# Optimization experiments

Measured on AMD Instinct MI355X. Metric: run time of the kernel, lower is better.

The kernel has to match this reference:

```python
import jax, jax.numpy as jnp
import numpy as np

B, S, D = 128, 512, 768          # batch, seq_len, token_dim
NH, HD = 8, 96                    # num_heads, head_dim = sentence_dim/num_heads
HID = 4 * HD                      # hidden_dim = 384


def setup_inputs() -> dict:
    key = jax.random.key(0)
    ks = jax.random.split(key, 9)
    token_embeddings = jax.random.normal(ks[0], (B, S, D), dtype=jnp.float32)
    # variable-length attention mask (1 for real tokens, 0 for padding)
    lengths = jax.random.randint(ks[1], (B,), S // 2, S + 1)
    attention_mask = (jnp.arange(S)[None, :] < lengths[:, None]).astype(jnp.float32)
    s = 0.02
    P  = jax.random.normal(ks[2], (NH, HD, D),   dtype=jnp.float32) * s
    bP = jnp.zeros((NH, HD), dtype=jnp.float32)
    W1 = jax.random.normal(ks[3], (NH, HID, HD), dtype=jnp.float32) * s
    b1 = jnp.zeros((NH, HID), dtype=jnp.float32)
    W2 = jax.random.normal(ks[4], (NH, HD, HID), dtype=jnp.float32) * s
    b2 = jnp.zeros((NH, HD), dtype=jnp.float32)
    return {"token_embeddings": token_embeddings, "attention_mask": attention_mask,
            "P": P, "bP": bP, "W1": W1, "b1": b1, "W2": W2, "b2": b2}


def reference(token_embeddings, attention_mask, P, bP, W1, b1, W2, b2):
    # per-head projection: H_i = P_i(H)           -> (nh, B, S, HD)
    Hi = jnp.einsum('bsd,ihd->ibsh', token_embeddings, P) + bP[:, None, None, :]
    # scores: W2(relu(W1(H_i)))                   -> (nh, B, S, HD)
    A = jnp.einsum('ibsf,ihf->ibsh',
                   jax.nn.relu(jnp.einsum('ibsh,ifh->ibsf', Hi, W1) + b1[:, None, None, :]),
                   W2) + b2[:, None, None, :]
    # masked softmax over sequence dim (log(mask) adds -inf on padding)
    log_mask = jnp.log(attention_mask)[None, :, :, None]  # (1, B, S, 1)
    A = jax.nn.softmax(A + log_mask, axis=2)
    # weighted sum over tokens                    -> (nh, B, HD)
    v = jnp.sum(Hi * A, axis=2)
    # concat heads: (B, nh*HD) = (B, 768)
    pooled = jnp.transpose(v, (1, 0, 2)).reshape(token_embeddings.shape[0], NH * HD)
    return pooled
```

## Files before the change

### kernel.cpp

```cpp
#include <hip/hip_runtime.h>
#include <stdint.h>


typedef short bf16x8 __attribute__((ext_vector_type(8)));
typedef float f32x4 __attribute__((ext_vector_type(4)));

struct alignas(8) us4 { unsigned short x, y, z, w; };

__device__ __forceinline__ unsigned short f32_to_bf16(float f) {
  union { float f; uint32_t u; } v; v.f = f;
  uint32_t u = v.u;
  uint32_t r = (u + 0x7fffu + ((u >> 16) & 1u)) >> 16;
  return (unsigned short)r;
}

__device__ __forceinline__ float bf16_to_f32(unsigned short h) {
  union { uint32_t u; float f; } v; v.u = ((uint32_t)h) << 16;
  return v.f;
}

__device__ __forceinline__ uint32_t pack_bf16_trunc(float lo, float hi) {
  union { float f; uint32_t u; } a, b; a.f = lo; b.f = hi;
  return __builtin_amdgcn_perm(b.u, a.u, 0x07060302u);
}

__device__ __forceinline__ void g2l16(const unsigned short* g, unsigned short* l) {
  __builtin_amdgcn_global_load_lds((__attribute__((address_space(1))) void*)g,
                                   (__attribute__((address_space(3))) void*)l,
                                   16, 0, 0);
}


#define N_X   50331648
#define N_P   589824
#define N_W1  294912
#define N_W2  294912
#define N_HI  50331648


__global__ __launch_bounds__(256) void cast_f32_bf16(
    const float* __restrict__ src, unsigned short* __restrict__ dst, int n4) {
  int idx = blockIdx.x * 256 + threadIdx.x;
  if (idx >= n4) return;
  float4 v = ((const float4*)src)[idx];
  us4 o;
  o.x = f32_to_bf16(v.x);
  o.y = f32_to_bf16(v.y);
  o.z = f32_to_bf16(v.z);
  o.w = f32_to_bf16(v.w);
  ((us4*)dst)[idx] = o;
}


__global__ __launch_bounds__(256) void gemm_hi(
    const unsigned short* __restrict__ Xbf,
    const unsigned short* __restrict__ Pbf,
    const float* __restrict__ bP,
    unsigned short* __restrict__ Hi) {
  __shared__ __align__(16) unsigned short As[128 * 32];
  __shared__ __align__(16) unsigned short Bs[128 * 32];

  const int tid = threadIdx.x;
  const int w = tid >> 6;
  const int lane = tid & 63;
  const int r = lane & 15;
  const int q = lane >> 4;
  const int bn = blockIdx.x;
  const int bm = blockIdx.y;
  const int wr = w >> 1, wc = w & 1;

  f32x4 acc[4][4];
#pragma unroll
  for (int a = 0; a < 4; ++a)
#pragma unroll
    for (int c = 0; c < 4; ++c) acc[a][c] = (f32x4){0.f, 0.f, 0.f, 0.f};

  const int ldr = lane >> 2;
  const int ldc = (lane & 3) * 8;
  const unsigned short* Abase = Xbf + (size_t)(bm * 128) * 768 + ldc;
  const unsigned short* Bbase = Pbf + (size_t)(bn * 128) * 768 + ldc;

  for (int k0 = 0; k0 < 768; k0 += 32) {
    __syncthreads();
    g2l16(Abase + (size_t)(w * 16 + ldr) * 768 + k0, &As[w * 512]);
    g2l16(Abase + (size_t)(64 + w * 16 + ldr) * 768 + k0, &As[(4 + w) * 512]);
    g2l16(Bbase + (size_t)(w * 16 + ldr) * 768 + k0, &Bs[w * 512]);
    g2l16(Bbase + (size_t)(64 + w * 16 + ldr) * 768 + k0, &Bs[(4 + w) * 512]);
    __syncthreads();

    bf16x8 af[4], bfr[4];
#pragma unroll
    for (int t = 0; t < 4; ++t)
      af[t] = *(const bf16x8*)&As[(wr * 64 + t * 16 + r) * 32 + q * 8];
#pragma unroll
    for (int t = 0; t < 4; ++t)
      bfr[t] = *(const bf16x8*)&Bs[(wc * 64 + t * 16 + r) * 32 + q * 8];
#pragma unroll
    for (int mt = 0; mt < 4; ++mt)
#pragma unroll
      for (int nt = 0; nt < 4; ++nt)
        acc[mt][nt] = __builtin_amdgcn_mfma_f32_16x16x32_bf16(
            af[mt], bfr[nt], acc[mt][nt], 0, 0, 0);
  }

  const int bb = bm >> 2;
  const int sb = (bm & 3) * 128 + wr * 64;
#pragma unroll
  for (int nt = 0; nt < 4; ++nt) {
    const int n0 = bn * 128 + wc * 64 + nt * 16;
    const int hd = n0 / 96;
    const int h = n0 - hd * 96 + r;
    const float bias = bP[n0 + r];
    unsigned short* obase = Hi + (size_t)(hd * 128 + bb) * 512 * 96 + h;
#pragma unroll
    for (int mt = 0; mt < 4; ++mt) {
#pragma unroll
      for (int rg = 0; rg < 4; ++rg) {
        const int s = sb + mt * 16 + q * 4 + rg;
        obase[(size_t)s * 96] = f32_to_bf16(acc[mt][nt][rg] + bias);
      }
    }
  }
}


__global__ __launch_bounds__(256, 2) void mlp_logits(
    const unsigned short* __restrict__ Hi,
    const unsigned short* __restrict__ W1bf,
    const unsigned short* __restrict__ W2bf,
    const float* __restrict__ b1,
    const float* __restrict__ b2,
    unsigned short* __restrict__ Alog) {
  __shared__ __align__(16) unsigned short Ys[128 * 96];
  __shared__ __align__(16) unsigned short Ws[96 * 96];
  __shared__ __align__(16) unsigned short Fs[128 * 104];
  __shared__ __align__(16) float b1s[384];
  __shared__ __align__(16) float b2s[96];

  const int x = blockIdx.x;
  const int c = x & 3;
  const int b = (x >> 2) & 127;
  const int hd = x >> 9;

  const int tid = threadIdx.x;
  const int w = tid >> 6;
  const int lane = tid & 63;
  const int r = lane & 15;
  const int q = lane >> 4;

  const unsigned short* ysrc = Hi + ((size_t)(hd * 128 + b) * 512 + c * 128) * 96;
#pragma unroll
  for (int it = 0; it < 6; ++it)
    g2l16(ysrc + (size_t)((it * 4 + w) * 64 + lane) * 8, &Ys[(it * 4 + w) * 512]);

  if (tid < 96) b2s[tid] = b2[hd * 96 + tid];
  for (int i = tid; i < 384; i += 256) b1s[i] = b1[hd * 384 + i];

  f32x4 acc3[2][6];
#pragma unroll
  for (int sp = 0; sp < 2; ++sp)
#pragma unroll
    for (int nt = 0; nt < 6; ++nt) acc3[sp][nt] = (f32x4){0.f, 0.f, 0.f, 0.f};

  for (int ph = 0; ph < 4; ++ph) {
    __syncthreads();
    const unsigned short* w1src = W1bf + ((size_t)hd * 384 + ph * 96) * 96;
#pragma unroll
    for (int it = 0; it < 4; ++it)
      g2l16(w1src + (size_t)((it * 4 + w) * 64 + lane) * 8, &Ws[(it * 4 + w) * 512]);
    if (w < 2)
      g2l16(w1src + (size_t)((16 + w) * 64 + lane) * 8, &Ws[(16 + w) * 512]);
    __syncthreads();

    f32x4 acc2[6][2];
#pragma unroll
    for (int ft = 0; ft < 6; ++ft)
#pragma unroll
      for (int sp = 0; sp < 2; ++sp) acc2[ft][sp] = (f32x4){0.f, 0.f, 0.f, 0.f};
#pragma unroll
    for (int kb = 0; kb < 3; ++kb) {
      bf16x8 bfrg[2];
#pragma unroll
      for (int sp = 0; sp < 2; ++sp)
        bfrg[sp] = *(const bf16x8*)&Ys[((w * 2 + sp) * 16 + r) * 96 + kb * 32 + q * 8];
#pragma unroll
      for (int ft = 0; ft < 6; ++ft) {
        bf16x8 afrg = *(const bf16x8*)&Ws[(ft * 16 + r) * 96 + kb * 32 + q * 8];
#pragma unroll
        for (int sp = 0; sp < 2; ++sp)
          acc2[ft][sp] = __builtin_amdgcn_mfma_f32_16x16x32_bf16(
              afrg, bfrg[sp], acc2[ft][sp], 0, 0, 0);
      }
    }
#pragma unroll
    for (int ft = 0; ft < 6; ++ft) {
      float4 bv = *(const float4*)&b1s[ph * 96 + ft * 16 + q * 4];
#pragma unroll
      for (int sp = 0; sp < 2; ++sp) {
        const int s = (w * 2 + sp) * 16 + r;
        float v0 = fmaxf(acc2[ft][sp][0] + bv.x, 0.f);
        float v1 = fmaxf(acc2[ft][sp][1] + bv.y, 0.f);
        float v2 = fmaxf(acc2[ft][sp][2] + bv.z, 0.f);
        float v3 = fmaxf(acc2[ft][sp][3] + bv.w, 0.f);
        uint2 pk;
        pk.x = pack_bf16_trunc(v0, v1);
        pk.y = pack_bf16_trunc(v2, v3);
        *(uint2*)((uint32_t*)&Fs[0] + s * 52 + ft * 8 + q * 2) = pk;
      }
    }
    __syncthreads();

    const unsigned short* w2src = W2bf + (size_t)hd * 96 * 384 + ph * 96;
#pragma unroll
    for (int it = 0; it < 4; ++it) {
      const int ch = (it * 4 + w) * 64 + lane;
      const int kb = ch / 384;
      const int rem = ch - kb * 384;
      g2l16(w2src + (size_t)(rem >> 2) * 384 + kb * 32 + (rem & 3) * 8,
            &Ws[(it * 4 + w) * 512]);
    }
    if (w < 2) {
      const int ch = (16 + w) * 64 + lane;
      const int kb = ch / 384;
      const int rem = ch - kb * 384;
      g2l16(w2src + (size_t)(rem >> 2) * 384 + kb * 32 + (rem & 3) * 8,
            &Ws[(16 + w) * 512]);
    }
    __syncthreads();

#pragma unroll
    for (int kb = 0; kb < 3; ++kb) {
      bf16x8 afrg[2];
#pragma unroll
      for (int sp = 0; sp < 2; ++sp)
        afrg[sp] = *(const bf16x8*)&Fs[((w * 2 + sp) * 16 + r) * 104 + kb * 32 + q * 8];
#pragma unroll
      for (int nt = 0; nt < 6; ++nt) {
        bf16x8 bfrg = *(const bf16x8*)&Ws[(kb * 96 + nt * 16 + r) * 32 + q * 8];
#pragma unroll
        for (int sp = 0; sp < 2; ++sp)
          acc3[sp][nt] = __builtin_amdgcn_mfma_f32_16x16x32_bf16(
              afrg[sp], bfrg, acc3[sp][nt], 0, 0, 0);
      }
    }
  }

  unsigned short* aout = Alog + ((size_t)(hd * 128 + b) * 512 + c * 128) * 96;
#pragma unroll
  for (int nt = 0; nt < 6; ++nt) {
    const int h = nt * 16 + r;
    const float bias = b2s[h];
#pragma unroll
    for (int sp = 0; sp < 2; ++sp) {
#pragma unroll
      for (int rg = 0; rg < 4; ++rg) {
        const int s = (w * 2 + sp) * 16 + q * 4 + rg;
        aout[(size_t)s * 96 + h] = f32_to_bf16(acc3[sp][nt][rg] + bias);
      }
    }
  }
}


__global__ __launch_bounds__(384) void softpool(
    const unsigned short* __restrict__ Hi,
    const unsigned short* __restrict__ Alog,
    const float* __restrict__ mask,
    float* __restrict__ out) {
  __shared__ float bias[512];
  __shared__ float redl[32][96];
  __shared__ float redv[32][96];
  __shared__ float mfin[96];

  const int x = blockIdx.x;
  const int hd = x >> 7;
  const int b = x & 127;
  const int tid = threadIdx.x;
  const int g = tid / 12;
  const int t12 = tid - g * 12;
  const int h8 = t12 * 8;

  for (int s = tid; s < 512; s += 384)
    bias[s] = mask[b * 512 + s] > 0.5f ? 0.f : -1e30f;
  __syncthreads();

  const unsigned short* abase = Alog + (size_t)x * 512 * 96;
  const unsigned short* hbase = Hi + (size_t)x * 512 * 96;

  float m[8];
#pragma unroll
  for (int j = 0; j < 8; ++j) m[j] = -3e30f;
#pragma unroll
  for (int it = 0; it < 16; ++it) {
    const int s = g * 16 + it;
    bf16x8 a = *(const bf16x8*)&abase[(size_t)s * 96 + h8];
    const float bs = bias[s];
#pragma unroll
    for (int j = 0; j < 8; ++j)
      m[j] = fmaxf(m[j], bf16_to_f32((unsigned short)a[j]) + bs);
  }
#pragma unroll
  for (int j = 0; j < 8; ++j) redl[g][h8 + j] = m[j];
  __syncthreads();
  if (tid < 96) {
    float mm = -3e30f;
#pragma unroll
    for (int gg = 0; gg < 32; ++gg) mm = fmaxf(mm, redl[gg][tid]);
    mfin[tid] = mm;
  }
  __syncthreads();
  float mf[8];
#pragma unroll
  for (int j = 0; j < 8; ++j) mf[j] = mfin[h8 + j];
  __syncthreads();

  float l[8], v[8];
#pragma unroll
  for (int j = 0; j < 8; ++j) { l[j] = 0.f; v[j] = 0.f; }
#pragma unroll
  for (int it = 0; it < 16; ++it) {
    const int s = g * 16 + it;
    bf16x8 a = *(const bf16x8*)&abase[(size_t)s * 96 + h8];
    bf16x8 hv = *(const bf16x8*)&hbase[(size_t)s * 96 + h8];
    const float bs = bias[s];
#pragma unroll
    for (int j = 0; j < 8; ++j) {
      float e = __expf(bf16_to_f32((unsigned short)a[j]) + bs - mf[j]);
      l[j] += e;
      v[j] += e * bf16_to_f32((unsigned short)hv[j]);
    }
  }
#pragma unroll
  for (int j = 0; j < 8; ++j) {
    redl[g][h8 + j] = l[j];
    redv[g][h8 + j] = v[j];
  }
  __syncthreads();
  if (tid < 96) {
    float ls = 0.f, vs = 0.f;
#pragma unroll
    for (int gg = 0; gg < 32; ++gg) { ls += redl[gg][tid]; vs += redv[gg][tid]; }
    out[b * 768 + hd * 96 + tid] = vs / ls;
  }
}


extern "C" void kernel_launch(void* const* d_in, const int* in_sizes, int n_in,
                              void* d_out, int out_size, void* d_ws, size_t ws_size,
                              hipStream_t stream) {
  const float* X    = (const float*)d_in[0];
  const float* mask = (const float*)d_in[1];
  const float* P    = (const float*)d_in[2];
  const float* bP   = (const float*)d_in[3];
  const float* W1   = (const float*)d_in[4];
  const float* b1   = (const float*)d_in[5];
  const float* W2   = (const float*)d_in[6];
  const float* b2   = (const float*)d_in[7];
  float* out = (float*)d_out;
  (void)in_sizes; (void)n_in; (void)out_size; (void)ws_size;

  unsigned short* Xbf  = (unsigned short*)d_ws;
  unsigned short* Pbf  = Xbf + N_X;
  unsigned short* W1bf = Pbf + N_P;
  unsigned short* W2bf = W1bf + N_W1;
  unsigned short* Hi   = W2bf + N_W2;
  unsigned short* Alog = Hi + N_HI;

  cast_f32_bf16<<<N_X / 4 / 256, 256, 0, stream>>>(X, Xbf, N_X / 4);
  cast_f32_bf16<<<N_P / 4 / 256, 256, 0, stream>>>(P, Pbf, N_P / 4);
  cast_f32_bf16<<<N_W1 / 4 / 256, 256, 0, stream>>>(W1, W1bf, N_W1 / 4);
  cast_f32_bf16<<<N_W2 / 4 / 256, 256, 0, stream>>>(W2, W2bf, N_W2 / 4);

  gemm_hi<<<dim3(6, 512), 256, 0, stream>>>(Xbf, Pbf, bP, Hi);
  mlp_logits<<<8 * 128 * 4, 256, 0, stream>>>(Hi, W1bf, W2bf, b1, b2, Alog);
  softpool<<<8 * 128, 384, 0, stream>>>(Hi, Alog, mask, out);
}
```

Measured before the change: 581.0 us.

## Keep MLP intermediate in registers via ds_bpermute, drop LDS staging and syncs

Rewrites mlp_logits so the Hi tile, W1 and W2 fragments are loaded directly from global memory into registers rather than staged through shared memory. The ReLU hidden activations are passed from the first MFMA output layout into the second MFMA input layout with ds_bpermute lane shuffles instead of an LDS round trip. This removes all __syncthreads and shared memory from the kernel and raises the occupancy hint to 3 blocks per CU. The output store is also reworked to write packed 4-element bf16 vectors along the head dim. In exchange, weights are re-read from global/L2 by every wave, with more, smaller loads and higher register pressure.

```diff
diff --git a/kernel.cpp b/kernel.cpp
--- a/kernel.cpp
+++ b/kernel.cpp
@@ -124,19 +124,13 @@
 }
 
 
-__global__ __launch_bounds__(256, 2) void mlp_logits(
+__global__ __launch_bounds__(256, 3) void mlp_logits(
     const unsigned short* __restrict__ Hi,
     const unsigned short* __restrict__ W1bf,
     const unsigned short* __restrict__ W2bf,
     const float* __restrict__ b1,
     const float* __restrict__ b2,
     unsigned short* __restrict__ Alog) {
-  __shared__ __align__(16) unsigned short Ys[128 * 96];
-  __shared__ __align__(16) unsigned short Ws[96 * 96];
-  __shared__ __align__(16) unsigned short Fs[128 * 104];
-  __shared__ __align__(16) float b1s[384];
-  __shared__ __align__(16) float b2s[96];
-
   const int x = blockIdx.x;
   const int c = x & 3;
   const int b = (x >> 2) & 127;
@@ -148,13 +142,23 @@
   const int r = lane & 15;
   const int q = lane >> 4;
 
-  const unsigned short* ysrc = Hi + ((size_t)(hd * 128 + b) * 512 + c * 128) * 96;
-#pragma unroll
-  for (int it = 0; it < 6; ++it)
-    g2l16(ysrc + (size_t)((it * 4 + w) * 64 + lane) * 8, &Ys[(it * 4 + w) * 512]);
-
-  if (tid < 96) b2s[tid] = b2[hd * 96 + tid];
-  for (int i = tid; i < 384; i += 256) b1s[i] = b1[hd * 384 + i];
+  const unsigned short* ybase = Hi + ((size_t)(hd * 128 + b) * 512 + c * 128) * 96;
+  const unsigned short* w1h = W1bf + (size_t)hd * 384 * 96;
+  const unsigned short* w2h = W2bf + (size_t)hd * 96 * 384;
+  const float* b1h = b1 + hd * 384;
+  const float* b2h = b2 + hd * 96;
+
+  bf16x8 yf[2][3];
+#pragma unroll
+  for (int sp = 0; sp < 2; ++sp)
+#pragma unroll
+    for (int kb = 0; kb < 3; ++kb)
+      yf[sp][kb] =
+          *(const bf16x8*)&ybase[((w * 2 + sp) * 16 + r) * 96 + kb * 32 + q * 8];
+
+  const int vaddr_a = (((lane >> 4) & 1) * 32 + r) * 4;
+  const int vaddr_b = vaddr_a + 64;
+  const bool hiq = lane >= 32;
 
   f32x4 acc3[2][6];
 #pragma unroll
@@ -163,100 +167,77 @@
     for (int nt = 0; nt < 6; ++nt) acc3[sp][nt] = (f32x4){0.f, 0.f, 0.f, 0.f};
 
   for (int ph = 0; ph < 4; ++ph) {
-    __syncthreads();
-    const unsigned short* w1src = W1bf + ((size_t)hd * 384 + ph * 96) * 96;
-#pragma unroll
-    for (int it = 0; it < 4; ++it)
-      g2l16(w1src + (size_t)((it * 4 + w) * 64 + lane) * 8, &Ws[(it * 4 + w) * 512]);
-    if (w < 2)
-      g2l16(w1src + (size_t)((16 + w) * 64 + lane) * 8, &Ws[(16 + w) * 512]);
-    __syncthreads();
-
-    f32x4 acc2[6][2];
-#pragma unroll
-    for (int ft = 0; ft < 6; ++ft)
-#pragma unroll
-      for (int sp = 0; sp < 2; ++sp) acc2[ft][sp] = (f32x4){0.f, 0.f, 0.f, 0.f};
-#pragma unroll
-    for (int kb = 0; kb < 3; ++kb) {
-      bf16x8 bfrg[2];
-#pragma unroll
-      for (int sp = 0; sp < 2; ++sp)
-        bfrg[sp] = *(const bf16x8*)&Ys[((w * 2 + sp) * 16 + r) * 96 + kb * 32 + q * 8];
-#pragma unroll
-      for (int ft = 0; ft < 6; ++ft) {
-        bf16x8 afrg = *(const bf16x8*)&Ws[(ft * 16 + r) * 96 + kb * 32 + q * 8];
-#pragma unroll
-        for (int sp = 0; sp < 2; ++sp)
-          acc2[ft][sp] = __builtin_amdgcn_mfma_f32_16x16x32_bf16(
-              afrg, bfrg[sp], acc2[ft][sp], 0, 0, 0);
+#pragma unroll
+    for (int kb2 = 0; kb2 < 3; ++kb2) {
+      uint32_t PX[2][2], PY[2][2];
+#pragma unroll
+      for (int fh = 0; fh < 2; ++fh) {
+        const int ft = kb2 * 2 + fh;
+        const int frow = ph * 96 + ft * 16 + r;
+        f32x4 a2[2];
+        a2[0] = (f32x4){0.f, 0.f, 0.f, 0.f};
+        a2[1] = (f32x4){0.f, 0.f, 0.f, 0.f};
+#pragma unroll
+        for (int kb = 0; kb < 3; ++kb) {
+          bf16x8 w1f = *(const bf16x8*)&w1h[(size_t)frow * 96 + kb * 32 + q * 8];
+#pragma unroll
+          for (int sp = 0; sp < 2; ++sp)
+            a2[sp] = __builtin_amdgcn_mfma_f32_16x16x32_bf16(w1f, yf[sp][kb],
+                                                             a2[sp], 0, 0, 0);
+        }
+        const float4 bv = *(const float4*)&b1h[ph * 96 + ft * 16 + q * 4];
+#pragma unroll
+        for (int sp = 0; sp < 2; ++sp) {
+          float v0 = fmaxf(a2[sp][0] + bv.x, 0.f);
+          float v1 = fmaxf(a2[sp][1] + bv.y, 0.f);
+          float v2 = fmaxf(a2[sp][2] + bv.z, 0.f);
+          float v3 = fmaxf(a2[sp][3] + bv.w, 0.f);
+          PX[fh][sp] = pack_bf16_trunc(v0, v1);
+          PY[fh][sp] = pack_bf16_trunc(v2, v3);
+        }
+      }
+      bf16x8 w2f[6];
+#pragma unroll
+      for (int nt = 0; nt < 6; ++nt)
+        w2f[nt] = *(const bf16x8*)&w2h[(size_t)(nt * 16 + r) * 384 + ph * 96 +
+                                       kb2 * 32 + q * 8];
+#pragma unroll
+      for (int sp = 0; sp < 2; ++sp) {
+        union { bf16x8 v; uint32_t d[4]; } bb;
+        uint32_t t0, t1;
+        t0 = (uint32_t)__builtin_amdgcn_ds_bpermute(vaddr_a, (int)PX[0][sp]);
+        t1 = (uint32_t)__builtin_amdgcn_ds_bpermute(vaddr_a, (int)PX[1][sp]);
+        bb.d[0] = hiq ? t1 : t0;
+        t0 = (uint32_t)__builtin_amdgcn_ds_bpermute(vaddr_a, (int)PY[0][sp]);
+        t1 = (uint32_t)__builtin_amdgcn_ds_bpermute(vaddr_a, (int)PY[1][sp]);
+        bb.d[1] = hiq ? t1 : t0;
+        t0 = (uint32_t)__builtin_amdgcn_ds_bpermute(vaddr_b, (int)PX[0][sp]);
+        t1 = (uint32_t)__builtin_amdgcn_ds_bpermute(vaddr_b, (int)PX[1][sp]);
+        bb.d[2] = hiq ? t1 : t0;
+        t0 = (uint32_t)__builtin_amdgcn_ds_bpermute(vaddr_b, (int)PY[0][sp]);
+        t1 = (uint32_t)__builtin_amdgcn_ds_bpermute(vaddr_b, (int)PY[1][sp]);
+        bb.d[3] = hiq ? t1 : t0;
+#pragma unroll
+        for (int nt = 0; nt < 6; ++nt)
+          acc3[sp][nt] = __builtin_amdgcn_mfma_f32_16x16x32_bf16(
+              w2f[nt], bb.v, acc3[sp][nt], 0, 0, 0);
       }
     }
-#pragma unroll
-    for (int ft = 0; ft < 6; ++ft) {
-      float4 bv = *(const float4*)&b1s[ph * 96 + ft * 16 + q * 4];
-#pragma unroll
-      for (int sp = 0; sp < 2; ++sp) {
-        const int s = (w * 2 + sp) * 16 + r;
-        float v0 = fmaxf(acc2[ft][sp][0] + bv.x, 0.f);
-        float v1 = fmaxf(acc2[ft][sp][1] + bv.y, 0.f);
-        float v2 = fmaxf(acc2[ft][sp][2] + bv.z, 0.f);
-        float v3 = fmaxf(acc2[ft][sp][3] + bv.w, 0.f);
-        uint2 pk;
-        pk.x = pack_bf16_trunc(v0, v1);
-        pk.y = pack_bf16_trunc(v2, v3);
-        *(uint2*)((uint32_t*)&Fs[0] + s * 52 + ft * 8 + q * 2) = pk;
-      }
-    }
-    __syncthreads();
-
-    const unsigned short* w2src = W2bf + (size_t)hd * 96 * 384 + ph * 96;
-#pragma unroll
-    for (int it = 0; it < 4; ++it) {
-      const int ch = (it * 4 + w) * 64 + lane;
-      const int kb = ch / 384;
-      const int rem = ch - kb * 384;
-      g2l16(w2src + (size_t)(rem >> 2) * 384 + kb * 32 + (rem & 3) * 8,
-            &Ws[(it * 4 + w) * 512]);
-    }
-    if (w < 2) {
-      const int ch = (16 + w) * 64 + lane;
-      const int kb = ch / 384;
-      const int rem = ch - kb * 384;
-      g2l16(w2src + (size_t)(rem >> 2) * 384 + kb * 32 + (rem & 3) * 8,
-            &Ws[(16 + w) * 512]);
-    }
-    __syncthreads();
-
-#pragma unroll
-    for (int kb = 0; kb < 3; ++kb) {
-      bf16x8 afrg[2];
-#pragma unroll
-      for (int sp = 0; sp < 2; ++sp)
-        afrg[sp] = *(const bf16x8*)&Fs[((w * 2 + sp) * 16 + r) * 104 + kb * 32 + q * 8];
-#pragma unroll
-      for (int nt = 0; nt < 6; ++nt) {
-        bf16x8 bfrg = *(const bf16x8*)&Ws[(kb * 96 + nt * 16 + r) * 32 + q * 8];
-#pragma unroll
-        for (int sp = 0; sp < 2; ++sp)
-          acc3[sp][nt] = __builtin_amdgcn_mfma_f32_16x16x32_bf16(
-              afrg[sp], bfrg, acc3[sp][nt], 0, 0, 0);
-      }
-    }
   }
 
   unsigned short* aout = Alog + ((size_t)(hd * 128 + b) * 512 + c * 128) * 96;
 #pragma unroll
   for (int nt = 0; nt < 6; ++nt) {
-    const int h = nt * 16 + r;
-    const float bias = b2s[h];
+    const float4 bv = *(const float4*)&b2h[nt * 16 + q * 4];
 #pragma unroll
     for (int sp = 0; sp < 2; ++sp) {
-#pragma unroll
-      for (int rg = 0; rg < 4; ++rg) {
-        const int s = (w * 2 + sp) * 16 + q * 4 + rg;
-        aout[(size_t)s * 96 + h] = f32_to_bf16(acc3[sp][nt][rg] + bias);
-      }
+      const int s = (w * 2 + sp) * 16 + r;
+      uint2 pk;
+      pk.x = (uint32_t)f32_to_bf16(acc3[sp][nt][0] + bv.x) |
+             ((uint32_t)f32_to_bf16(acc3[sp][nt][1] + bv.y) << 16);
+      pk.y = (uint32_t)f32_to_bf16(acc3[sp][nt][2] + bv.z) |
+             ((uint32_t)f32_to_bf16(acc3[sp][nt][3] + bv.w) << 16);
+      *(uint2*)&aout[(size_t)s * 96 + nt * 16 + q * 4] = pk;
     }
   }
 }
```

New measurement: 699.0 us. +20.3%, slower.
